# Optimization experiments

Hardware: AMD Instinct MI355X
Metric: run time of the kernel (lower is better)

Reference implementation:

```python
import jax, jax.numpy as jnp
import numpy as np

D_MODEL = 1024
N_HEADS = 16
D_HEAD = D_MODEL // N_HEADS


def setup_inputs() -> dict:
    key = jax.random.key(0)
    k_x, k_wqkv, k_bqkv, k_wo, k_bo = jax.random.split(key, 5)
    B, S = 2, 2048
    x = jax.random.normal(k_x, (B, S, D_MODEL), dtype=jnp.float32)
    # torch Linear: y = x @ W.T + b; store W as [out, in] like torch
    bound1 = 1.0 / np.sqrt(D_MODEL)
    W_qkv = jax.random.uniform(k_wqkv, (3 * D_MODEL, D_MODEL), minval=-bound1, maxval=bound1, dtype=jnp.float32)
    b_qkv = jax.random.uniform(k_bqkv, (3 * D_MODEL,), minval=-bound1, maxval=bound1, dtype=jnp.float32)
    W_out = jax.random.uniform(k_wo, (D_MODEL, D_MODEL), minval=-bound1, maxval=bound1, dtype=jnp.float32)
    b_out = jax.random.uniform(k_bo, (D_MODEL,), minval=-bound1, maxval=bound1, dtype=jnp.float32)
    return {"x": x, "W_qkv": W_qkv, "b_qkv": b_qkv, "W_out": W_out, "b_out": b_out}


def reference(x, W_qkv, b_qkv, W_out, b_out):
    B, S, D = x.shape
    qkv = x @ W_qkv.T + b_qkv                       # [B, S, 3D]
    qkv = qkv.reshape(B, S, 3, N_HEADS, D_HEAD)
    qkv = jnp.transpose(qkv, (2, 0, 3, 1, 4))       # [3, B, H, S, Dh]
    q, k, v = qkv[0], qkv[1], qkv[2]
    scores = jnp.einsum('bhqd,bhkd->bhqk', q, k) / np.sqrt(D_HEAD).astype(np.float32)
    causal = jnp.tril(jnp.ones((S, S), dtype=bool))
    scores = jnp.where(causal[None, None], scores, jnp.float32(-jnp.inf))
    attn = jax.nn.softmax(scores, axis=-1)          # dropout p=0 -> identity
    out = jnp.einsum('bhqk,bhkd->bhqd', attn, v)    # [B, H, S, Dh]
    out = jnp.transpose(out, (0, 2, 1, 3)).reshape(B, S, D)
    return out @ W_out.T + b_out
```

## Files before the change

### kernel.cpp

```cpp
#include <hip/hip_runtime.h>
#include <hip/hip_bf16.h>
#include <cstdint>


#define DEV __device__ __forceinline__

#define VT_STRIDE 2048
#define QSCALE 0.1803368801f

using bf16x8 = __attribute__((ext_vector_type(8))) short;
using f32x4  = __attribute__((ext_vector_type(4))) float;
using f32x16 = __attribute__((ext_vector_type(16))) float;
using u32x4  = __attribute__((ext_vector_type(4))) unsigned;

DEV unsigned short f2bf(float f) {
  unsigned u = __builtin_bit_cast(unsigned, f);
  u = (u + 0x7fffu + ((u >> 16) & 1u)) >> 16;
  return (unsigned short)u;
}

DEV float exp2_hw(float x) {
  float r;
  asm("v_exp_f32 %0, %1" : "=v"(r) : "v"(x));
  return r;
}

typedef __attribute__((address_space(1))) unsigned int as1_uint;
typedef __attribute__((address_space(3))) unsigned int as3_uint;

DEV void gload_lds16(const void* g, void* l) {
  __builtin_amdgcn_global_load_lds(
      (as1_uint*)(uintptr_t)g,
      (as3_uint*)(unsigned int)(uintptr_t)l,
      16, 0, 0);
}

#define N4_X  (4096 * 1024 / 4)
#define N4_WQ (3072 * 1024 / 4)
#define N4_WO (1024 * 1024 / 4)
__global__ __launch_bounds__(256) void cvt_all_k(const float* __restrict__ x,
                                                 const float* __restrict__ wq,
                                                 const float* __restrict__ wo,
                                                 unsigned short* __restrict__ xb,
                                                 unsigned short* __restrict__ wqb,
                                                 unsigned short* __restrict__ wob) {
  int i = blockIdx.x * 256 + threadIdx.x;
  const float* in; unsigned short* out;
  if (i < N4_X)                { in = x;  out = xb; }
  else if (i < N4_X + N4_WQ)   { i -= N4_X;  in = wq; out = wqb; }
  else                         { i -= N4_X + N4_WQ; in = wo; out = wob; }
  float4 v = reinterpret_cast<const float4*>(in)[i];
  ushort4 o;
  o.x = f2bf(v.x); o.y = f2bf(v.y); o.z = f2bf(v.z); o.w = f2bf(v.w);
  reinterpret_cast<ushort4*>(out)[i] = o;
}

__global__ __launch_bounds__(256) void transpose_v_k(const unsigned short* __restrict__ V,
                                                     unsigned short* __restrict__ Vt) {
  const int bh = blockIdx.x;
  const int st = blockIdx.y;
  const int tid = threadIdx.x;
  __shared__ unsigned short T[64 * 64];
  const unsigned short* src = V + ((size_t)bh * 2048 + st * 64) * 64;

#pragma unroll
  for (int it = 0; it < 2; ++it) {
    const int c = it * 256 + tid;
    const int L = c * 16;
    const int S = L ^ (((L >> 10) & 7) << 4);
    gload_lds16((const char*)src + S, (char*)T + L);
  }
  __syncthreads();

#pragma unroll
  for (int it = 0; it < 2; ++it) {
    const int c = it * 256 + tid;
    const int d = c >> 3;
    const int s_off = (c & 7) * 8;
    const int xg = (c & 7) << 4;
    bf16x8 pk;
#pragma unroll
    for (int j = 0; j < 8; ++j)
      pk[j] = *(const short*)((const char*)T + (((s_off + j) * 128 + d * 2) ^ xg));
    *(bf16x8*)(Vt + (size_t)(bh * 64 + d) * VT_STRIDE + st * 64 + s_off) = pk;
  }
}

template <int MODE, int N, int K>
__global__ __launch_bounds__(256) void gemm_bt(const unsigned short* __restrict__ A,
                                               const unsigned short* __restrict__ W,
                                               const float* __restrict__ bias,
                                               float* __restrict__ Cout,
                                               unsigned short* __restrict__ Qp,
                                               unsigned short* __restrict__ Kp,
                                               unsigned short* __restrict__ Vp) {
  __shared__ unsigned short As[2][128 * 64];
  __shared__ unsigned short Bs[2][128 * 64];
  const int tid = threadIdx.x;
  const int m0 = blockIdx.x * 128;
  const int n0 = blockIdx.y * 128;
  const int w = tid >> 6, lane = tid & 63, g = lane >> 4, lr = lane & 15;
  const int wr = w >> 1, wc = w & 1;
  const int xr = (lr & 7) << 4;

  f32x4 acc[4][4];
#pragma unroll
  for (int i = 0; i < 4; ++i)
#pragma unroll
    for (int j = 0; j < 4; ++j)
#pragma unroll
      for (int r = 0; r < 4; ++r) acc[i][j][r] = 0.f;

#define GSTAGE(buf, kt)                                                                     \
  do {                                                                                      \
    _Pragma("unroll")                                                                       \
    for (int it = 0; it < 4; ++it) {                                                        \
      const int c = it * 256 + tid;                                                         \
      const int row = c >> 3;                                                               \
      const int colb = ((c & 7) * 16) ^ ((row & 7) << 4);                                   \
      gload_lds16((const char*)(A + (size_t)(m0 + row) * K + (kt)) + colb,                  \
                  (char*)As[buf] + c * 16);                                                 \
      gload_lds16((const char*)(W + (size_t)(n0 + row) * K + (kt)) + colb,                  \
                  (char*)Bs[buf] + c * 16);                                                 \
    }                                                                                       \
  } while (0)

  GSTAGE(0, 0);
  int cur = 0;
  const int nsteps = K / 64;
  for (int step = 0; step < nsteps; ++step) {
    if (step + 1 < nsteps) {
      GSTAGE(cur ^ 1, (step + 1) * 64);
      asm volatile("s_waitcnt vmcnt(8)" ::: "memory");
    } else {
      asm volatile("s_waitcnt vmcnt(0)" ::: "memory");
    }
    __builtin_amdgcn_s_barrier();
    __builtin_amdgcn_sched_barrier(0);

    const char* AsC = (const char*)As[cur];
    const char* BsC = (const char*)Bs[cur];
    __builtin_amdgcn_s_setprio(1);
#pragma unroll
    for (int ks = 0; ks < 2; ++ks) {
      bf16x8 af[4], bf[4];
#pragma unroll
      for (int mi = 0; mi < 4; ++mi)
        af[mi] = *(const bf16x8*)(AsC +
                   ((((wr * 64 + mi * 16 + lr) * 128) + ks * 64 + g * 16) ^ xr));
#pragma unroll
      for (int ni = 0; ni < 4; ++ni)
        bf[ni] = *(const bf16x8*)(BsC +
                   ((((wc * 64 + ni * 16 + lr) * 128) + ks * 64 + g * 16) ^ xr));
#pragma unroll
      for (int mi = 0; mi < 4; ++mi)
#pragma unroll
        for (int ni = 0; ni < 4; ++ni)
          acc[mi][ni] = __builtin_amdgcn_mfma_f32_16x16x32_bf16(af[mi], bf[ni], acc[mi][ni], 0, 0, 0);
    }
    __builtin_amdgcn_s_setprio(0);

    asm volatile("" ::: "memory");
    __builtin_amdgcn_s_barrier();
    __builtin_amdgcn_sched_barrier(0);
    cur ^= 1;
  }
#undef GSTAGE

  if (MODE == 0) {
#pragma unroll
    for (int ni = 0; ni < 4; ++ni) {
      const int col = n0 + wc * 64 + ni * 16 + lr;
      const float bv = bias[col];
#pragma unroll
      for (int mi = 0; mi < 4; ++mi)
#pragma unroll
        for (int r = 0; r < 4; ++r) {
          const int row = m0 + wr * 64 + mi * 16 + g * 4 + r;
          Cout[(size_t)row * N + col] = acc[mi][ni][r] + bv;
        }
    }
  } else {
#pragma unroll
    for (int ni = 0; ni < 4; ++ni) {
      const int col = n0 + wc * 64 + ni * 16 + lr;
      const float bv = bias[col];
      const int which = col >> 10;
      const int h = (col >> 6) & 15;
      const int d = col & 63;
      unsigned short* P = which == 0 ? Qp : which == 1 ? Kp : Vp;
      const float scl = which == 0 ? QSCALE : 1.0f;
#pragma unroll
      for (int mi = 0; mi < 4; ++mi)
#pragma unroll
        for (int r = 0; r < 4; ++r) {
          const int row = m0 + wr * 64 + mi * 16 + g * 4 + r;
          const int b = row >> 11, s = row & 2047;
          P[(((size_t)(b * 16 + h) * 2048 + s) << 6) + d] = f2bf((acc[mi][ni][r] + bv) * scl);
        }
    }
  }
}

__global__ __launch_bounds__(128) void attn_fwd(const unsigned short* __restrict__ Q,
                                                const unsigned short* __restrict__ Kg,
                                                const unsigned short* __restrict__ Vt,
                                                unsigned short* __restrict__ AO) {
  const int bh = blockIdx.x;
  const int qt = 31 - blockIdx.y;
  const int tid = threadIdx.x;
  const int w = tid >> 6, lane = tid & 63;
  const int l31 = lane & 31, hi = lane >> 5;
  const int xr = (lane & 7) << 4;
  const unsigned short* Qp = Q  + (size_t)bh * 2048 * 64;
  const unsigned short* Kp = Kg + (size_t)bh * 2048 * 64;
  const unsigned short* Vp = Vt + (size_t)bh * 64 * VT_STRIDE;
  const int b = bh >> 4, h = bh & 15;

  __shared__ unsigned short Ks[2][64 * 64];
  __shared__ unsigned short Vs[2][64 * 64];

#define STAGE(buf, kvb)                                                                     \
  do {                                                                                      \
    _Pragma("unroll")                                                                       \
    for (int it = 0; it < 4; ++it) {                                                        \
      const int Lc = (it * 128 + tid) * 16;                                                 \
      const int Gc = Lc ^ (((Lc >> 7) & 7) << 4);                                           \
      gload_lds16((const char*)Kp + (size_t)(kvb) * 128 + Gc, (char*)Ks[buf] + Lc);         \
      gload_lds16((const char*)Vp + (size_t)(Gc >> 7) * (VT_STRIDE * 2) +                   \
                      (size_t)(kvb) * 2 + (Gc & 127), (char*)Vs[buf] + Lc);                 \
    }                                                                                       \
  } while (0)

  const int nb = qt + 1;
  const int qrow0 = qt * 64 + w * 32;

  STAGE(0, 0);
  int cur = 0;

  bf16x8 qf[4];
#pragma unroll
  for (int ds = 0; ds < 4; ++ds)
    qf[ds] = *(const bf16x8*)(Qp + (size_t)(qrow0 + l31) * 64 + ds * 16 + hi * 8);

  f32x16 o0, o1;
#pragma unroll
  for (int r = 0; r < 16; ++r) { o0[r] = 0.f; o1[r] = 0.f; }
  float lp = 0.f;

  for (int t = 0; t < nb; ++t) {
    const int kvb = t * 64;
    if (t + 1 < nb) {
      STAGE(cur ^ 1, (t + 1) * 64);
      asm volatile("s_waitcnt vmcnt(8)" ::: "memory");
    } else {
      asm volatile("s_waitcnt vmcnt(0)" ::: "memory");
    }
    __builtin_amdgcn_s_barrier();
    __builtin_amdgcn_sched_barrier(0);

    const char* KsC = (const char*)Ks[cur];
    const char* VsC = (const char*)Vs[cur];

    f32x16 s0, s1;
#pragma unroll
    for (int r = 0; r < 16; ++r) { s0[r] = 0.f; s1[r] = 0.f; }
    __builtin_amdgcn_s_setprio(1);
#pragma unroll
    for (int ds = 0; ds < 4; ++ds) {
      bf16x8 k0 = *(const bf16x8*)(KsC + ((l31 * 128 + ds * 32 + hi * 16) ^ xr));
      bf16x8 k1 = *(const bf16x8*)(KsC + (((32 + l31) * 128 + ds * 32 + hi * 16) ^ xr));
      s0 = __builtin_amdgcn_mfma_f32_32x32x16_bf16(k0, qf[ds], s0, 0, 0, 0);
      s1 = __builtin_amdgcn_mfma_f32_32x32x16_bf16(k1, qf[ds], s1, 0, 0, 0);
    }
    __builtin_amdgcn_s_setprio(0);

    if (t == nb - 1) {
      const int thr = w * 32 + l31;
#pragma unroll
      for (int reg = 0; reg < 16; ++reg) {
        const int koff = (reg & 3) + 8 * (reg >> 2) + 4 * hi;
        if (koff > thr)      s0[reg] = -INFINITY;
        if (koff + 32 > thr) s1[reg] = -INFINITY;
      }
    }

#pragma unroll
    for (int reg = 0; reg < 16; ++reg) {
      float a0 = exp2_hw(s0[reg]);
      float a1 = exp2_hw(s1[reg]);
      s0[reg] = a0; s1[reg] = a1;
      lp += a0 + a1;
    }

    bf16x8 pa[4];
#pragma unroll
    for (int kb = 0; kb < 2; ++kb) {
      unsigned wv[8], tv[8];
#pragma unroll
      for (int j = 0; j < 8; ++j) {
        float e0 = kb ? s1[2 * j] : s0[2 * j];
        float e1 = kb ? s1[2 * j + 1] : s0[2 * j + 1];
        asm("v_cvt_pk_bf16_f32 %0, %1, %2" : "=v"(wv[j]) : "v"(e0), "v"(e1));
      }
#pragma unroll
      for (int j = 0; j < 8; ++j) tv[j] = (unsigned)__shfl_xor((int)wv[j], 32);
      u32x4 ua, ub;
      ua[0] = hi ? tv[2] : wv[0]; ua[1] = hi ? tv[3] : wv[1];
      ua[2] = hi ? wv[2] : tv[0]; ua[3] = hi ? wv[3] : tv[1];
      ub[0] = hi ? tv[6] : wv[4]; ub[1] = hi ? tv[7] : wv[5];
      ub[2] = hi ? wv[6] : tv[4]; ub[3] = hi ? wv[7] : tv[5];
      pa[kb * 2]     = __builtin_bit_cast(bf16x8, ua);
      pa[kb * 2 + 1] = __builtin_bit_cast(bf16x8, ub);
    }

    __builtin_amdgcn_s_setprio(1);
#pragma unroll
    for (int ks = 0; ks < 4; ++ks) {
      bf16x8 v0 = *(const bf16x8*)(VsC + ((l31 * 128 + ks * 32 + hi * 16) ^ xr));
      bf16x8 v1 = *(const bf16x8*)(VsC + (((32 + l31) * 128 + ks * 32 + hi * 16) ^ xr));
      o0 = __builtin_amdgcn_mfma_f32_32x32x16_bf16(pa[ks], v0, o0, 0, 0, 0);
      o1 = __builtin_amdgcn_mfma_f32_32x32x16_bf16(pa[ks], v1, o1, 0, 0, 0);
    }
    __builtin_amdgcn_s_setprio(0);

    asm volatile("" ::: "memory");
    __builtin_amdgcn_s_barrier();
    __builtin_amdgcn_sched_barrier(0);
    cur ^= 1;
  }

  lp += __shfl_xor(lp, 32);
  const float inv = 1.0f / lp;
#pragma unroll
  for (int reg = 0; reg < 16; ++reg) {
    const int qoff = (reg & 3) + 8 * (reg >> 2) + 4 * hi;
    const float li = __shfl(inv, qoff);
    const int row = qrow0 + qoff;
    AO[(size_t)(b * 2048 + row) * 1024 + h * 64 + l31]      = f2bf(o0[reg] * li);
    AO[(size_t)(b * 2048 + row) * 1024 + h * 64 + 32 + l31] = f2bf(o1[reg] * li);
  }
#undef STAGE
}

extern "C" void kernel_launch(void* const* d_in, const int* in_sizes, int n_in,
                              void* d_out, int out_size, void* d_ws, size_t ws_size,
                              hipStream_t stream) {
  const float* x     = (const float*)d_in[0];
  const float* W_qkv = (const float*)d_in[1];
  const float* b_qkv = (const float*)d_in[2];
  const float* W_out = (const float*)d_in[3];
  const float* b_out = (const float*)d_in[4];
  float* out = (float*)d_out;

  char* ws = (char*)d_ws;
  unsigned short* xb  = (unsigned short*)(ws);
  unsigned short* AOb = (unsigned short*)(ws);
  unsigned short* wqb = (unsigned short*)(ws + ((size_t)8 << 20));
  unsigned short* wob = (unsigned short*)(ws + ((size_t)14 << 20));
  unsigned short* Qb  = (unsigned short*)(ws + ((size_t)16 << 20));
  unsigned short* Kb  = (unsigned short*)(ws + ((size_t)24 << 20));
  unsigned short* Vb  = (unsigned short*)(ws + ((size_t)32 << 20));
  unsigned short* Vtb = (unsigned short*)(ws + ((size_t)40 << 20));

  cvt_all_k<<<(N4_X + N4_WQ + N4_WO) / 256, 256, 0, stream>>>(x, W_qkv, W_out, xb, wqb, wob);

  gemm_bt<1, 3072, 1024><<<dim3(32, 24), 256, 0, stream>>>(xb, wqb, b_qkv, nullptr, Qb, Kb, Vb);
  transpose_v_k<<<dim3(32, 32), 256, 0, stream>>>(Vb, Vtb);
  attn_fwd<<<dim3(32, 32), 128, 0, stream>>>(Qb, Kb, Vtb, AOb);
  gemm_bt<0, 1024, 1024><<<dim3(32, 8), 256, 0, stream>>>(AOb, wob, b_out, out, nullptr, nullptr, nullptr);
}
```

Baseline: 116.4 us.

## Split long causal attention rows across KV chunks with atomic accumulation

Causal query tiles at qt>=8 are split into chunks of up to 8 KV blocks, each handled by its own block. Partial unnormalized outputs and row sums are added into fp32 buffers with atomics, and a new combine kernel normalizes them and writes bf16. This targets the load imbalance of long causal rows and aims to fill more CUs. In exchange it adds a zero kernel, a combine kernel, atomic traffic, and drops the double-buffered K/V prefetch for a simpler single-buffer loop with full syncthreads. The softmax needs no max-rescaling because scores are used without subtracting a running max, so the partial sums add directly.

```diff
diff --git a/kernel.cpp b/kernel.cpp
--- a/kernel.cpp
+++ b/kernel.cpp
@@ -55,35 +55,26 @@
   reinterpret_cast<ushort4*>(out)[i] = o;
 }
 
-__global__ __launch_bounds__(256) void transpose_v_k(const unsigned short* __restrict__ V,
-                                                     unsigned short* __restrict__ Vt) {
-  const int bh = blockIdx.x;
-  const int st = blockIdx.y;
-  const int tid = threadIdx.x;
-  __shared__ unsigned short T[64 * 64];
-  const unsigned short* src = V + ((size_t)bh * 2048 + st * 64) * 64;
-
-#pragma unroll
-  for (int it = 0; it < 2; ++it) {
-    const int c = it * 256 + tid;
-    const int L = c * 16;
-    const int S = L ^ (((L >> 10) & 7) << 4);
-    gload_lds16((const char*)src + S, (char*)T + L);
-  }
-  __syncthreads();
-
-#pragma unroll
-  for (int it = 0; it < 2; ++it) {
-    const int c = it * 256 + tid;
-    const int d = c >> 3;
-    const int s_off = (c & 7) * 8;
-    const int xg = (c & 7) << 4;
-    bf16x8 pk;
-#pragma unroll
-    for (int j = 0; j < 8; ++j)
-      pk[j] = *(const short*)((const char*)T + (((s_off + j) * 128 + d * 2) ^ xg));
-    *(bf16x8*)(Vt + (size_t)(bh * 64 + d) * VT_STRIDE + st * 64 + s_off) = pk;
-  }
+__global__ __launch_bounds__(256) void zero_k(float4* __restrict__ p) {
+  const float4 z = {0.f, 0.f, 0.f, 0.f};
+  p[blockIdx.x * 256 + threadIdx.x] = z;
+}
+
+__global__ __launch_bounds__(256) void combine_k(const float* __restrict__ Oacc,
+                                                 const float* __restrict__ lacc,
+                                                 unsigned short* __restrict__ AO) {
+  const int i = blockIdx.x * 256 + threadIdx.x;
+  const int d4 = i & 15;
+  const int rem = i >> 4;
+  const int row = rem % 1536;
+  const int bh = rem / 1536;
+  const float inv = 1.0f / lacc[rem];
+  float4 v = reinterpret_cast<const float4*>(Oacc)[i];
+  const int b = bh >> 4, h = bh & 15;
+  ushort4 u;
+  u.x = f2bf(v.x * inv); u.y = f2bf(v.y * inv);
+  u.z = f2bf(v.z * inv); u.w = f2bf(v.w * inv);
+  *(ushort4*)(AO + ((size_t)(b * 2048 + 512 + row)) * 1024 + h * 64 + d4 * 4) = u;
 }
 
 template <int MODE, int N, int K>
@@ -202,12 +193,50 @@
   }
 }
 
+__global__ __launch_bounds__(256) void transpose_v_k(const unsigned short* __restrict__ V,
+                                                     unsigned short* __restrict__ Vt) {
+  const int bh = blockIdx.x;
+  const int st = blockIdx.y;
+  const int tid = threadIdx.x;
+  __shared__ unsigned short T[64 * 64];
+  const unsigned short* src = V + ((size_t)bh * 2048 + st * 64) * 64;
+
+#pragma unroll
+  for (int it = 0; it < 2; ++it) {
+    const int c = it * 256 + tid;
+    const int L = c * 16;
+    const int S = L ^ (((L >> 10) & 7) << 4);
+    gload_lds16((const char*)src + S, (char*)T + L);
+  }
+  __syncthreads();
+
+#pragma unroll
+  for (int it = 0; it < 2; ++it) {
+    const int c = it * 256 + tid;
+    const int d = c >> 3;
+    const int s_off = (c & 7) * 8;
+    const int xg = (c & 7) << 4;
+    bf16x8 pk;
+#pragma unroll
+    for (int j = 0; j < 8; ++j)
+      pk[j] = *(const short*)((const char*)T + (((s_off + j) * 128 + d * 2) ^ xg));
+    *(bf16x8*)(Vt + (size_t)(bh * 64 + d) * VT_STRIDE + st * 64 + s_off) = pk;
+  }
+}
+
 __global__ __launch_bounds__(128) void attn_fwd(const unsigned short* __restrict__ Q,
                                                 const unsigned short* __restrict__ Kg,
                                                 const unsigned short* __restrict__ Vt,
-                                                unsigned short* __restrict__ AO) {
+                                                unsigned short* __restrict__ AO,
+                                                float* __restrict__ Oacc,
+                                                float* __restrict__ lacc) {
   const int bh = blockIdx.x;
-  const int qt = 31 - blockIdx.y;
+  int yy = blockIdx.y, qt = 0, c = 0;
+  for (int qq = 31; qq >= 0; --qq) {
+    const int n = (qq >> 3) + 1;
+    if (yy < n) { qt = qq; c = yy; break; }
+    yy -= n;
+  }
   const int tid = threadIdx.x;
   const int w = tid >> 6, lane = tid & 63;
   const int l31 = lane & 31, hi = lane >> 5;
@@ -217,26 +246,25 @@
   const unsigned short* Vp = Vt + (size_t)bh * 64 * VT_STRIDE;
   const int b = bh >> 4, h = bh & 15;
 
-  __shared__ unsigned short Ks[2][64 * 64];
-  __shared__ unsigned short Vs[2][64 * 64];
-
-#define STAGE(buf, kvb)                                                                     \
+  __shared__ unsigned short Ks[64 * 64];
+  __shared__ unsigned short Vs[64 * 64];
+
+#define STAGE(kvb)                                                                          \
   do {                                                                                      \
     _Pragma("unroll")                                                                       \
     for (int it = 0; it < 4; ++it) {                                                        \
       const int Lc = (it * 128 + tid) * 16;                                                 \
       const int Gc = Lc ^ (((Lc >> 7) & 7) << 4);                                           \
-      gload_lds16((const char*)Kp + (size_t)(kvb) * 128 + Gc, (char*)Ks[buf] + Lc);         \
+      gload_lds16((const char*)Kp + (size_t)(kvb) * 128 + Gc, (char*)Ks + Lc);              \
       gload_lds16((const char*)Vp + (size_t)(Gc >> 7) * (VT_STRIDE * 2) +                   \
-                      (size_t)(kvb) * 2 + (Gc & 127), (char*)Vs[buf] + Lc);                 \
+                      (size_t)(kvb) * 2 + (Gc & 127), (char*)Vs + Lc);                      \
     }                                                                                       \
   } while (0)
 
-  const int nb = qt + 1;
+  const int kv0 = c * 8;
+  const int nbl = min(8, qt + 1 - kv0);
+  const bool split = (qt >= 8);
   const int qrow0 = qt * 64 + w * 32;
-
-  STAGE(0, 0);
-  int cur = 0;
 
   bf16x8 qf[4];
 #pragma unroll
@@ -248,19 +276,10 @@
   for (int r = 0; r < 16; ++r) { o0[r] = 0.f; o1[r] = 0.f; }
   float lp = 0.f;
 
-  for (int t = 0; t < nb; ++t) {
-    const int kvb = t * 64;
-    if (t + 1 < nb) {
-      STAGE(cur ^ 1, (t + 1) * 64);
-      asm volatile("s_waitcnt vmcnt(8)" ::: "memory");
-    } else {
-      asm volatile("s_waitcnt vmcnt(0)" ::: "memory");
-    }
-    __builtin_amdgcn_s_barrier();
-    __builtin_amdgcn_sched_barrier(0);
-
-    const char* KsC = (const char*)Ks[cur];
-    const char* VsC = (const char*)Vs[cur];
+  for (int tl = 0; tl < nbl; ++tl) {
+    const int tglob = kv0 + tl;
+    STAGE(tglob * 64);
+    __syncthreads();
 
     f32x16 s0, s1;
 #pragma unroll
@@ -268,14 +287,14 @@
     __builtin_amdgcn_s_setprio(1);
 #pragma unroll
     for (int ds = 0; ds < 4; ++ds) {
-      bf16x8 k0 = *(const bf16x8*)(KsC + ((l31 * 128 + ds * 32 + hi * 16) ^ xr));
-      bf16x8 k1 = *(const bf16x8*)(KsC + (((32 + l31) * 128 + ds * 32 + hi * 16) ^ xr));
+      bf16x8 k0 = *(const bf16x8*)((const char*)Ks + ((l31 * 128 + ds * 32 + hi * 16) ^ xr));
+      bf16x8 k1 = *(const bf16x8*)((const char*)Ks + (((32 + l31) * 128 + ds * 32 + hi * 16) ^ xr));
       s0 = __builtin_amdgcn_mfma_f32_32x32x16_bf16(k0, qf[ds], s0, 0, 0, 0);
       s1 = __builtin_amdgcn_mfma_f32_32x32x16_bf16(k1, qf[ds], s1, 0, 0, 0);
     }
     __builtin_amdgcn_s_setprio(0);
 
-    if (t == nb - 1) {
+    if (tglob == qt) {
       const int thr = w * 32 + l31;
 #pragma unroll
       for (int reg = 0; reg < 16; ++reg) {
@@ -317,28 +336,38 @@
     __builtin_amdgcn_s_setprio(1);
 #pragma unroll
     for (int ks = 0; ks < 4; ++ks) {
-      bf16x8 v0 = *(const bf16x8*)(VsC + ((l31 * 128 + ks * 32 + hi * 16) ^ xr));
-      bf16x8 v1 = *(const bf16x8*)(VsC + (((32 + l31) * 128 + ks * 32 + hi * 16) ^ xr));
+      bf16x8 v0 = *(const bf16x8*)((const char*)Vs + ((l31 * 128 + ks * 32 + hi * 16) ^ xr));
+      bf16x8 v1 = *(const bf16x8*)((const char*)Vs + (((32 + l31) * 128 + ks * 32 + hi * 16) ^ xr));
       o0 = __builtin_amdgcn_mfma_f32_32x32x16_bf16(pa[ks], v0, o0, 0, 0, 0);
       o1 = __builtin_amdgcn_mfma_f32_32x32x16_bf16(pa[ks], v1, o1, 0, 0, 0);
     }
     __builtin_amdgcn_s_setprio(0);
 
-    asm volatile("" ::: "memory");
-    __builtin_amdgcn_s_barrier();
-    __builtin_amdgcn_sched_barrier(0);
-    cur ^= 1;
+    __syncthreads();
   }
 
   lp += __shfl_xor(lp, 32);
-  const float inv = 1.0f / lp;
-#pragma unroll
-  for (int reg = 0; reg < 16; ++reg) {
-    const int qoff = (reg & 3) + 8 * (reg >> 2) + 4 * hi;
-    const float li = __shfl(inv, qoff);
-    const int row = qrow0 + qoff;
-    AO[(size_t)(b * 2048 + row) * 1024 + h * 64 + l31]      = f2bf(o0[reg] * li);
-    AO[(size_t)(b * 2048 + row) * 1024 + h * 64 + 32 + l31] = f2bf(o1[reg] * li);
+
+  if (!split) {
+    const float inv = 1.0f / lp;
+#pragma unroll
+    for (int reg = 0; reg < 16; ++reg) {
+      const int qoff = (reg & 3) + 8 * (reg >> 2) + 4 * hi;
+      const float li = __shfl(inv, qoff);
+      const int row = qrow0 + qoff;
+      AO[(size_t)(b * 2048 + row) * 1024 + h * 64 + l31]      = f2bf(o0[reg] * li);
+      AO[(size_t)(b * 2048 + row) * 1024 + h * 64 + 32 + l31] = f2bf(o1[reg] * li);
+    }
+  } else {
+    if (hi == 0)
+      atomicAdd(&lacc[bh * 1536 + qrow0 - 512 + l31], lp);
+#pragma unroll
+    for (int reg = 0; reg < 16; ++reg) {
+      const int qoff = (reg & 3) + 8 * (reg >> 2) + 4 * hi;
+      const size_t base = ((size_t)bh * 1536 + (qrow0 + qoff - 512)) * 64;
+      atomicAdd(&Oacc[base + l31],      o0[reg]);
+      atomicAdd(&Oacc[base + 32 + l31], o1[reg]);
+    }
   }
 #undef STAGE
 }
@@ -355,18 +384,22 @@
 
   char* ws = (char*)d_ws;
   unsigned short* xb  = (unsigned short*)(ws);
-  unsigned short* AOb = (unsigned short*)(ws);
+  float*          Oacc= (float*)(ws);
   unsigned short* wqb = (unsigned short*)(ws + ((size_t)8 << 20));
-  unsigned short* wob = (unsigned short*)(ws + ((size_t)14 << 20));
-  unsigned short* Qb  = (unsigned short*)(ws + ((size_t)16 << 20));
-  unsigned short* Kb  = (unsigned short*)(ws + ((size_t)24 << 20));
-  unsigned short* Vb  = (unsigned short*)(ws + ((size_t)32 << 20));
+  float*          lacc= (float*)(ws + ((size_t)12 << 20));
+  unsigned short* Vb  = (unsigned short*)(ws + ((size_t)14 << 20));
+  unsigned short* AOb = (unsigned short*)(ws + ((size_t)14 << 20));
+  unsigned short* wob = (unsigned short*)(ws + ((size_t)22 << 20));
+  unsigned short* Qb  = (unsigned short*)(ws + ((size_t)24 << 20));
+  unsigned short* Kb  = (unsigned short*)(ws + ((size_t)32 << 20));
   unsigned short* Vtb = (unsigned short*)(ws + ((size_t)40 << 20));
 
   cvt_all_k<<<(N4_X + N4_WQ + N4_WO) / 256, 256, 0, stream>>>(x, W_qkv, W_out, xb, wqb, wob);
 
   gemm_bt<1, 3072, 1024><<<dim3(32, 24), 256, 0, stream>>>(xb, wqb, b_qkv, nullptr, Qb, Kb, Vb);
   transpose_v_k<<<dim3(32, 32), 256, 0, stream>>>(Vb, Vtb);
-  attn_fwd<<<dim3(32, 32), 128, 0, stream>>>(Qb, Kb, Vtb, AOb);
+  zero_k<<<798720 / 256, 256, 0, stream>>>((float4*)Oacc);
+  attn_fwd<<<dim3(32, 80), 128, 0, stream>>>(Qb, Kb, Vtb, AOb, Oacc, lacc);
+  combine_k<<<786432 / 256, 256, 0, stream>>>(Oacc, lacc, AOb);
   gemm_bt<0, 1024, 1024><<<dim3(32, 8), 256, 0, stream>>>(AOb, wob, b_out, out, nullptr, nullptr, nullptr);
 }
```

After: 129.1 us. 1.11x slower.
